# Performance work log

Measured on AMD Instinct MI355X. Metric: run time of the kernel, lower is better.

Reference implementation:

```python
import jax, jax.numpy as jnp
import numpy as np

N = 262144  # points per batch (~4096 rays x 64 samples)
FDIM = 64   # plane feature dim
S = 512     # base plane resolution


def setup_inputs() -> dict:
    key = jax.random.key(0)
    ks = jax.random.split(key, 10)
    x = jax.random.uniform(ks[0], (N, 3), dtype=jnp.float32, minval=-1.0, maxval=1.0)
    rays_o = jnp.array([[0.0, 0.0, 1.5]], dtype=jnp.float32)  # ray origin; distances straddle 1.5/2.0
    scale = jnp.ones((3,), dtype=jnp.float32)
    plane = lambda k, s: jax.random.normal(k, (FDIM, s, s), dtype=jnp.float32)
    return {
        'x': x, 'rays_o': rays_o, 'scale': scale,
        'xy_plane': plane(ks[1], S), 'yz_plane': plane(ks[2], S), 'xz_plane': plane(ks[3], S),
        'xy_plane1': plane(ks[4], S // 2), 'yz_plane1': plane(ks[5], S // 2), 'xz_plane1': plane(ks[6], S // 2),
        'xy_plane2': plane(ks[7], S // 4), 'yz_plane2': plane(ks[8], S // 4), 'xz_plane2': plane(ks[9], S // 4),
    }


def bilinear_sample(plane, coords):
    """F.grid_sample(mode='bilinear', align_corners=True, padding_mode='zeros').
    plane: [C, H, W]; coords: [N, 2] with (x, y) in [-1, 1] (x indexes W).
    Returns [N, C]."""
    C, H, W = plane.shape
    fx = (coords[:, 0] + 1.0) * 0.5 * (W - 1)
    fy = (coords[:, 1] + 1.0) * 0.5 * (H - 1)
    x0 = jnp.floor(fx)
    y0 = jnp.floor(fy)
    wx = fx - x0
    wy = fy - y0
    x0i = x0.astype(jnp.int32)
    y0i = y0.astype(jnp.int32)

    def gather(xi, yi):
        valid = (xi >= 0) & (xi < W) & (yi >= 0) & (yi < H)
        xc = jnp.clip(xi, 0, W - 1)
        yc = jnp.clip(yi, 0, H - 1)
        v = plane[:, yc, xc]  # [C, N]
        return jnp.where(valid[None, :], v, 0.0)

    v00 = gather(x0i, y0i)
    v01 = gather(x0i + 1, y0i)
    v10 = gather(x0i, y0i + 1)
    v11 = gather(x0i + 1, y0i + 1)
    out = (v00 * (1 - wx) * (1 - wy) + v01 * wx * (1 - wy)
           + v10 * (1 - wx) * wy + v11 * wx * wy)  # [C, N]
    return out.T


def forward(x, rays_o, scale, xy0, yz0, xz0, xy1, yz1, xz1, xy2, yz2, xz2):
    xs = x * scale[None, :]
    xy_c = xs[:, :2]                                   # (x, y)
    xz_c = jnp.stack([xs[:, 0], xs[:, 2]], axis=-1)    # (x, z)
    yz_c = xs[:, 1:]                                   # (y, z)

    # laplace breakpoints: first index with distance > 1.5 / > 2.0 from rays_o[0]
    d = jnp.linalg.norm(rays_o[0][None, :] - xs, axis=-1)
    c1 = d > 1.5
    c2 = d > 2.0
    break1 = jnp.where(c1.any(), jnp.argmax(c1), 0)
    break2 = jnp.where(c2.any(), jnp.argmax(c2), 0)
    idx = jnp.arange(x.shape[0])
    # level 0: [0, break1), level 1: [break1, break2), level 2: [break2, N)
    level = jnp.where(idx < break1, 0, jnp.where(idx < break2, 1, 2))[:, None]

    def tri(p0, p1, p2, c):
        s0 = bilinear_sample(p0, c)
        s1 = bilinear_sample(p1, c)
        s2 = bilinear_sample(p2, c)
        # laplace: level1 = fine + half, level2 = fine + half + quarter
        return jnp.where(level == 0, s0, jnp.where(level == 1, s0 + s1, s0 + s1 + s2))

    return (tri(xy0, xy1, xy2, xy_c)
            + tri(xz0, xz1, xz2, xz_c)
            + tri(yz0, yz1, yz2, yz_c))


def reference(x, rays_o, scale, xy_plane, yz_plane, xz_plane, xy_plane1, yz_plane1, xz_plane1, xy_plane2, yz_plane2, xz_plane2):
    return forward(x, rays_o, scale, xy_plane, yz_plane, xz_plane,
                   xy_plane1, yz_plane1, xz_plane1,
                   xy_plane2, yz_plane2, xz_plane2)
```

## Files before the change

kernel.cpp:

```cpp
#include <hip/hip_runtime.h>
#include <hip/hip_fp16.h>

#define NPTS 262144
#define FDIM 64
#define NCELL 4096

typedef float vfloat4 __attribute__((ext_vector_type(4)));

__global__ __launch_bounds__(256) void break_kernel(const float* __restrict__ x,
                                                    const float* __restrict__ rays_o,
                                                    const float* __restrict__ scale,
                                                    unsigned* __restrict__ breaks) {
  const unsigned t = blockIdx.x * 256u + threadIdx.x;
  const float r0 = rays_o[0], r1 = rays_o[1], r2 = rays_o[2];
  const float s0 = scale[0], s1 = scale[1], s2 = scale[2];
  unsigned b1 = 0xFFFFFFFFu, b2 = 0xFFFFFFFFu;
  for (unsigned p = t; p < NPTS; p += 65536u) {
    const float dx = r0 - x[p * 3 + 0] * s0;
    const float dy = r1 - x[p * 3 + 1] * s1;
    const float dz = r2 - x[p * 3 + 2] * s2;
    const float d = sqrtf(__fadd_rn(__fadd_rn(__fmul_rn(dx, dx), __fmul_rn(dy, dy)),
                                    __fmul_rn(dz, dz)));
    if (d > 1.5f) b1 = min(b1, p);
    if (d > 2.0f) b2 = min(b2, p);
  }
#pragma unroll
  for (int o = 32; o > 0; o >>= 1) {
    b1 = min(b1, (unsigned)__shfl_down((int)b1, o, 64));
    b2 = min(b2, (unsigned)__shfl_down((int)b2, o, 64));
  }
  if ((threadIdx.x & 63) == 0) {
    atomicMin(&breaks[0], b1);
    atomicMin(&breaks[1], b2);
  }
}

__device__ __forceinline__ unsigned part4(unsigned v) {
  v &= 15u;
  v = (v | (v << 4)) & 0x0C3u;
  v = (v | (v << 2)) & 0x249u;
  return v;
}

__device__ __forceinline__ unsigned cell_key(float x0, float x1, float x2) {
  const int cx = min(max((int)((x0 + 1.0f) * 8.0f), 0), 15);
  const int cy = min(max((int)((x1 + 1.0f) * 8.0f), 0), 15);
  const int cz = min(max((int)((x2 + 1.0f) * 8.0f), 0), 15);
  return part4((unsigned)cx) | (part4((unsigned)cy) << 1) | (part4((unsigned)cz) << 2);
}

#define NB_BH (NPTS / 256)
#define TPIX 128

struct TransposeArgs {
  const float* src[9];
  __half* dst[9];
  int tile_hi[9];
  int SS[9];
};

union H8 { uint4 u; __half h[8]; };

__global__ __launch_bounds__(256) void fused_bh_transpose(const float* __restrict__ x,
                                                          const float* __restrict__ rays_o,
                                                          const float* __restrict__ scale,
                                                          unsigned* __restrict__ breaks,
                                                          unsigned* __restrict__ hist,
                                                          TransposeArgs a) {
  const int bid = blockIdx.x;
  if (bid < NB_BH) {
    const unsigned t = (unsigned)bid * 256u + threadIdx.x;
    const float s0 = scale[0], s1 = scale[1], s2 = scale[2];
    const float xs0 = x[t * 3 + 0] * s0;
    const float xs1 = x[t * 3 + 1] * s1;
    const float xs2 = x[t * 3 + 2] * s2;
    const float dx = rays_o[0] - xs0;
    const float dy = rays_o[1] - xs1;
    const float dz = rays_o[2] - xs2;
    const float d = sqrtf(__fadd_rn(__fadd_rn(__fmul_rn(dx, dx), __fmul_rn(dy, dy)),
                                    __fmul_rn(dz, dz)));
    unsigned m1 = (d > 1.5f) ? (NPTS - t) : 0u;
    unsigned m2 = (d > 2.0f) ? (NPTS - t) : 0u;
#pragma unroll
    for (int o = 32; o > 0; o >>= 1) {
      m1 = max(m1, (unsigned)__shfl_down((int)m1, o, 64));
      m2 = max(m2, (unsigned)__shfl_down((int)m2, o, 64));
    }
    if ((threadIdx.x & 63) == 0) {
      atomicMax(&breaks[0], m1);
      atomicMax(&breaks[1], m2);
    }
    const unsigned key = cell_key(xs0, xs1, xs2);
    atomicAdd(&hist[key], 1u);
    return;
  }
  const int tile = bid - NB_BH;
  int pi = 0;
#pragma unroll
  for (int i = 0; i < 9; ++i) {
    if (tile >= a.tile_hi[i]) pi = i + 1;
  }
  const int lo = (pi == 0) ? 0 : a.tile_hi[pi - 1];
  const float* __restrict__ src = a.src[pi];
  __half* __restrict__ dst = a.dst[pi];
  const size_t SS = (size_t)a.SS[pi];

  const int ntm = (int)(SS / TPIX) - 1;
  const int tl = ((tile - lo) * 997) & ntm;

  const int t = threadIdx.x;
  const int slot = t >> 3;
  const int c8 = t & 7;
  const size_t p0 = (size_t)tl * TPIX + (size_t)slot * 4;
  const float* __restrict__ srcb = src + (size_t)(c8 * 8) * SS + p0;

  H8 h[4];
#pragma unroll
  for (int k = 0; k < 8; ++k) {
    const float4 v = *(const float4*)(srcb + (size_t)k * SS);
    h[0].h[k] = __float2half(v.x);
    h[1].h[k] = __float2half(v.y);
    h[2].h[k] = __float2half(v.z);
    h[3].h[k] = __float2half(v.w);
  }
#pragma unroll
  for (int r = 0; r < 4; ++r) {
    *(uint4*)(dst + (p0 + (size_t)r) * FDIM + c8 * 8) = h[r].u;
  }
}

__global__ __launch_bounds__(1024) void scan_kernel(unsigned* __restrict__ hist) {
  const int tid = threadIdx.x;
  uint4 h = ((uint4*)hist)[tid];
  const unsigned i0 = h.x;
  const unsigned i1 = i0 + h.y;
  const unsigned i2 = i1 + h.z;
  const unsigned i3 = i2 + h.w;
  __shared__ unsigned ls[1024];
  ls[tid] = i3;
  __syncthreads();
  for (int d = 1; d < 1024; d <<= 1) {
    const unsigned add = (tid >= d) ? ls[tid - d] : 0u;
    __syncthreads();
    ls[tid] += add;
    __syncthreads();
  }
  const unsigned base = ls[tid] - i3;
  uint4 o;
  o.x = base;
  o.y = base + i0;
  o.z = base + i1;
  o.w = base + i2;
  ((uint4*)hist)[tid] = o;
}

__global__ __launch_bounds__(256) void scatter_kernel(const float* __restrict__ x,
                                                      const float* __restrict__ scale,
                                                      const unsigned* __restrict__ breaks,
                                                      unsigned* __restrict__ offs,
                                                      unsigned* __restrict__ order) {
  const unsigned t = blockIdx.x * 256u + threadIdx.x;
  const float s0 = scale[0], s1 = scale[1], s2 = scale[2];
  const float xs0 = x[t * 3 + 0] * s0;
  const float xs1 = x[t * 3 + 1] * s1;
  const float xs2 = x[t * 3 + 2] * s2;
  const unsigned key = cell_key(xs0, xs1, xs2);
  const unsigned pos = atomicAdd(&offs[key], 1u);
  unsigned b1 = NPTS - breaks[0]; if (b1 >= NPTS) b1 = 0;
  unsigned b2 = NPTS - breaks[1]; if (b2 >= NPTS) b2 = 0;
  const unsigned lvl = (t < b1) ? 0u : ((t < b2) ? 1u : 2u);
  order[pos] = t | (lvl << 18);
}

__device__ __forceinline__ void bilinear_weights(int W, float cx, float cy,
                                                 float& w00, float& w01, float& w10, float& w11,
                                                 int& xc0, int& xc1, int& yc0, int& yc1) {
  const float Wm1 = (float)(W - 1);
  const float fx = (cx + 1.0f) * 0.5f * Wm1;
  const float fy = (cy + 1.0f) * 0.5f * Wm1;
  const float x0f = floorf(fx), y0f = floorf(fy);
  const float wx = fx - x0f, wy = fy - y0f;
  const int ix = (int)x0f, iy = (int)y0f;
  const int ix1 = ix + 1, iy1 = iy + 1;
  const bool vx0 = (ix >= 0) && (ix < W);
  const bool vx1 = (ix1 >= 0) && (ix1 < W);
  const bool vy0 = (iy >= 0) && (iy < W);
  const bool vy1 = (iy1 >= 0) && (iy1 < W);
  xc0 = min(max(ix, 0), W - 1);
  xc1 = min(max(ix1, 0), W - 1);
  yc0 = min(max(iy, 0), W - 1);
  yc1 = min(max(iy1, 0), W - 1);
  w00 = (1.0f - wx) * (1.0f - wy) * (float)(vx0 && vy0);
  w01 = wx * (1.0f - wy) * (float)(vx1 && vy0);
  w10 = (1.0f - wx) * wy * (float)(vx0 && vy1);
  w11 = wx * wy * (float)(vx1 && vy1);
}

__device__ __forceinline__ void sample8_t(const __half* __restrict__ pl, int W,
                                          float cx, float cy, int j8, float acc[8]) {
  float w00, w01, w10, w11;
  int xc0, xc1, yc0, yc1;
  bilinear_weights(W, cx, cy, w00, w01, w10, w11, xc0, xc1, yc0, yc1);
  const __half* b00 = pl + ((size_t)(yc0 * W + xc0) * FDIM + j8);
  const __half* b01 = pl + ((size_t)(yc0 * W + xc1) * FDIM + j8);
  const __half* b10 = pl + ((size_t)(yc1 * W + xc0) * FDIM + j8);
  const __half* b11 = pl + ((size_t)(yc1 * W + xc1) * FDIM + j8);
  H8 v00, v01, v10, v11;
  v00.u = *(const uint4*)b00;
  v01.u = *(const uint4*)b01;
  v10.u = *(const uint4*)b10;
  v11.u = *(const uint4*)b11;
#pragma unroll
  for (int k = 0; k < 8; ++k) {
    acc[k] += w00 * __half2float(v00.h[k]) + w01 * __half2float(v01.h[k]) +
              w10 * __half2float(v10.h[k]) + w11 * __half2float(v11.h[k]);
  }
}

__device__ __forceinline__ void sample8_d(const float* __restrict__ pl, int W,
                                          float cx, float cy, int j8, float acc[8]) {
  float w00, w01, w10, w11;
  int xc0, xc1, yc0, yc1;
  bilinear_weights(W, cx, cy, w00, w01, w10, w11, xc0, xc1, yc0, yc1);
  const size_t SS = (size_t)W * W;
  const int i00 = yc0 * W + xc0, i01 = yc0 * W + xc1;
  const int i10 = yc1 * W + xc0, i11 = yc1 * W + xc1;
#pragma unroll
  for (int k = 0; k < 8; ++k) {
    const size_t co = (size_t)(j8 + k) * SS;
    acc[k] += w00 * pl[co + i00] + w01 * pl[co + i01] +
              w10 * pl[co + i10] + w11 * pl[co + i11];
  }
}

struct PlanesH { const __half* p[9]; };
struct PlanesF { const float* p[9]; };

#define SAMPLE_BLOCKS (NPTS * 8 / 256)
#define XCD_CHUNK (SAMPLE_BLOCKS / 8)

__global__ __launch_bounds__(256) void sample_kernel(const float* __restrict__ x,
                                                     const float* __restrict__ scale,
                                                     const unsigned* __restrict__ order,
                                                     PlanesH tp, float* __restrict__ out) {
  const unsigned b = blockIdx.x;
  const unsigned sb = (b & 7u) * XCD_CHUNK + (b >> 3);
  const int t = (int)(sb * 256u + threadIdx.x);
  const int slot = t >> 3;
  const int j8 = (t & 7) * 8;
  const unsigned pk = order[slot];
  const int p = (int)(pk & 0x3FFFFu);
  const int level = (int)(pk >> 18);
  const float s0 = scale[0], s1 = scale[1], s2 = scale[2];
  const float xs0 = x[p * 3 + 0] * s0;
  const float xs1 = x[p * 3 + 1] * s1;
  const float xs2 = x[p * 3 + 2] * s2;
  float acc[8];
#pragma unroll
  for (int k = 0; k < 8; ++k) acc[k] = 0.0f;
  sample8_t(tp.p[0], 512, xs0, xs1, j8, acc);
  sample8_t(tp.p[1], 512, xs1, xs2, j8, acc);
  sample8_t(tp.p[2], 512, xs0, xs2, j8, acc);
  if (level >= 1) {
    sample8_t(tp.p[3], 256, xs0, xs1, j8, acc);
    sample8_t(tp.p[4], 256, xs1, xs2, j8, acc);
    sample8_t(tp.p[5], 256, xs0, xs2, j8, acc);
  }
  if (level >= 2) {
    sample8_t(tp.p[6], 128, xs0, xs1, j8, acc);
    sample8_t(tp.p[7], 128, xs1, xs2, j8, acc);
    sample8_t(tp.p[8], 128, xs0, xs2, j8, acc);
  }
  float* o = out + (size_t)p * FDIM + j8;
  vfloat4 lo = {acc[0], acc[1], acc[2], acc[3]};
  vfloat4 hi = {acc[4], acc[5], acc[6], acc[7]};
  __builtin_nontemporal_store(lo, (vfloat4*)o);
  __builtin_nontemporal_store(hi, (vfloat4*)(o + 4));
}

__global__ __launch_bounds__(256) void sample_kernel_direct(const float* __restrict__ x,
                                                            const float* __restrict__ scale,
                                                            const unsigned* __restrict__ breaks,
                                                            PlanesF tp, float* __restrict__ out) {
  const int t = blockIdx.x * 256 + threadIdx.x;
  const int p = t >> 3;
  const int j8 = (t & 7) * 8;
  const float s0 = scale[0], s1 = scale[1], s2 = scale[2];
  const float xs0 = x[p * 3 + 0] * s0;
  const float xs1 = x[p * 3 + 1] * s1;
  const float xs2 = x[p * 3 + 2] * s2;
  unsigned b1 = breaks[0]; if (b1 >= NPTS) b1 = 0;
  unsigned b2 = breaks[1]; if (b2 >= NPTS) b2 = 0;
  const unsigned pu = (unsigned)p;
  const int level = (pu < b1) ? 0 : ((pu < b2) ? 1 : 2);
  float acc[8];
#pragma unroll
  for (int k = 0; k < 8; ++k) acc[k] = 0.0f;
  sample8_d(tp.p[0], 512, xs0, xs1, j8, acc);
  sample8_d(tp.p[1], 512, xs1, xs2, j8, acc);
  sample8_d(tp.p[2], 512, xs0, xs2, j8, acc);
  if (level >= 1) {
    sample8_d(tp.p[3], 256, xs0, xs1, j8, acc);
    sample8_d(tp.p[4], 256, xs1, xs2, j8, acc);
    sample8_d(tp.p[5], 256, xs0, xs2, j8, acc);
  }
  if (level >= 2) {
    sample8_d(tp.p[6], 128, xs0, xs1, j8, acc);
    sample8_d(tp.p[7], 128, xs1, xs2, j8, acc);
    sample8_d(tp.p[8], 128, xs0, xs2, j8, acc);
  }
  float4* o4 = (float4*)(out + (size_t)p * FDIM + j8);
  o4[0] = make_float4(acc[0], acc[1], acc[2], acc[3]);
  o4[1] = make_float4(acc[4], acc[5], acc[6], acc[7]);
}

extern "C" void kernel_launch(void* const* d_in, const int* in_sizes, int n_in,
                              void* d_out, int out_size, void* d_ws, size_t ws_size,
                              hipStream_t stream) {
  const float* x = (const float*)d_in[0];
  const float* rays_o = (const float*)d_in[1];
  const float* scale = (const float*)d_in[2];
  const float* pl32[9];
  for (int i = 0; i < 9; ++i) pl32[i] = (const float*)d_in[3 + i];
  float* out = (float*)d_out;

  unsigned char* ws = (unsigned char*)d_ws;
  unsigned* breaks = (unsigned*)ws;
  unsigned* hist = (unsigned*)(ws + 256);
  unsigned* order = (unsigned*)(ws + 256 + NCELL * 4);
  const size_t planes_off = 256 + (size_t)NCELL * 4 + (size_t)NPTS * 4;

  const int Ss[3] = {512, 256, 128};
  size_t need = planes_off;
  for (int l = 0; l < 3; ++l) need += 3 * (size_t)Ss[l] * Ss[l] * FDIM * sizeof(__half);

  if (ws_size >= need) {
    (void)hipMemsetAsync(d_ws, 0, 256 + NCELL * 4, stream);

    PlanesH tp;
    TransposeArgs ta;
    size_t off = planes_off;
    int tiles_acc = 0;
    for (int l = 0; l < 3; ++l) {
      const int S = Ss[l];
      const int SS = S * S;
      for (int o = 0; o < 3; ++o) {
        const int i = l * 3 + o;
        __half* dst = (__half*)(ws + off);
        tp.p[i] = dst;
        ta.src[i] = pl32[i];
        ta.dst[i] = dst;
        ta.SS[i] = SS;
        tiles_acc += SS / TPIX;
        ta.tile_hi[i] = tiles_acc;
        off += (size_t)SS * FDIM * sizeof(__half);
      }
    }
    fused_bh_transpose<<<NB_BH + tiles_acc, 256, 0, stream>>>(x, rays_o, scale,
                                                              breaks, hist, ta);
    scan_kernel<<<1, 1024, 0, stream>>>(hist);
    scatter_kernel<<<NPTS / 256, 256, 0, stream>>>(x, scale, breaks, hist, order);
    sample_kernel<<<SAMPLE_BLOCKS, 256, 0, stream>>>(x, scale, order, tp, out);
  } else {
    (void)hipMemsetAsync(d_ws, 0xFF, 8, stream);
    break_kernel<<<256, 256, 0, stream>>>(x, rays_o, scale, breaks);
    PlanesF tf;
    for (int i = 0; i < 9; ++i) tf.p[i] = pl32[i];
    sample_kernel_direct<<<(NPTS * 8) / 256, 256, 0, stream>>>(x, scale, breaks, tf, out);
  }
}
```

Before: 474.9 us.

## Replace global-atomic counting sort with per-block LDS histograms and split transpose

The binning of points into Morton cells now uses 64 blocks, each building a shared-memory histogram and storing cell keys. A scan kernel sums the per-block histograms, prefix-scans them and writes per-block offsets. Scatter then reuses the stored keys and applies LDS atomics instead of global ones. The plane transpose is split out of the fused kernel into its own launch after the sort. This removes global atomic contention on the histogram, but the sort now runs on only 64 blocks and the serial scan over blocks lengthens the critical path.

```diff
diff --git a/kernel.cpp b/kernel.cpp
--- a/kernel.cpp
+++ b/kernel.cpp
@@ -4,6 +4,8 @@
 #define NPTS 262144
 #define FDIM 64
 #define NCELL 4096
+#define NBLK 64
+#define PPT 16
 
 typedef float vfloat4 __attribute__((ext_vector_type(4)));
 
@@ -49,93 +51,61 @@
   return part4((unsigned)cx) | (part4((unsigned)cy) << 1) | (part4((unsigned)cz) << 2);
 }
 
-#define NB_BH (NPTS / 256)
-#define TPIX 128
-
-struct TransposeArgs {
-  const float* src[9];
-  __half* dst[9];
-  int tile_hi[9];
-  int SS[9];
-};
-
-union H8 { uint4 u; __half h[8]; };
-
-__global__ __launch_bounds__(256) void fused_bh_transpose(const float* __restrict__ x,
-                                                          const float* __restrict__ rays_o,
-                                                          const float* __restrict__ scale,
-                                                          unsigned* __restrict__ breaks,
-                                                          unsigned* __restrict__ hist,
-                                                          TransposeArgs a) {
-  const int bid = blockIdx.x;
-  if (bid < NB_BH) {
-    const unsigned t = (unsigned)bid * 256u + threadIdx.x;
-    const float s0 = scale[0], s1 = scale[1], s2 = scale[2];
-    const float xs0 = x[t * 3 + 0] * s0;
-    const float xs1 = x[t * 3 + 1] * s1;
-    const float xs2 = x[t * 3 + 2] * s2;
-    const float dx = rays_o[0] - xs0;
-    const float dy = rays_o[1] - xs1;
-    const float dz = rays_o[2] - xs2;
+__global__ __launch_bounds__(256) void bh_hist_kernel(const float* __restrict__ x,
+                                                      const float* __restrict__ rays_o,
+                                                      const float* __restrict__ scale,
+                                                      unsigned* __restrict__ breaks,
+                                                      unsigned short* __restrict__ keys,
+                                                      unsigned* __restrict__ blockhist) {
+  __shared__ unsigned lh[NCELL];
+  for (int i = threadIdx.x; i < NCELL; i += 256) lh[i] = 0u;
+  __syncthreads();
+  const float r0 = rays_o[0], r1 = rays_o[1], r2 = rays_o[2];
+  const float s0 = scale[0], s1 = scale[1], s2 = scale[2];
+  const unsigned base = blockIdx.x * 256u + threadIdx.x;
+  unsigned m1 = 0u, m2 = 0u;
+#pragma unroll
+  for (int k = 0; k < PPT; ++k) {
+    const unsigned p = base + (unsigned)k * (NBLK * 256u);
+    const float xs0 = x[p * 3 + 0] * s0;
+    const float xs1 = x[p * 3 + 1] * s1;
+    const float xs2 = x[p * 3 + 2] * s2;
+    const float dx = r0 - xs0;
+    const float dy = r1 - xs1;
+    const float dz = r2 - xs2;
     const float d = sqrtf(__fadd_rn(__fadd_rn(__fmul_rn(dx, dx), __fmul_rn(dy, dy)),
                                     __fmul_rn(dz, dz)));
-    unsigned m1 = (d > 1.5f) ? (NPTS - t) : 0u;
-    unsigned m2 = (d > 2.0f) ? (NPTS - t) : 0u;
-#pragma unroll
-    for (int o = 32; o > 0; o >>= 1) {
-      m1 = max(m1, (unsigned)__shfl_down((int)m1, o, 64));
-      m2 = max(m2, (unsigned)__shfl_down((int)m2, o, 64));
-    }
-    if ((threadIdx.x & 63) == 0) {
-      atomicMax(&breaks[0], m1);
-      atomicMax(&breaks[1], m2);
-    }
+    if (d > 1.5f) m1 = max(m1, NPTS - p);
+    if (d > 2.0f) m2 = max(m2, NPTS - p);
     const unsigned key = cell_key(xs0, xs1, xs2);
-    atomicAdd(&hist[key], 1u);
-    return;
-  }
-  const int tile = bid - NB_BH;
-  int pi = 0;
-#pragma unroll
-  for (int i = 0; i < 9; ++i) {
-    if (tile >= a.tile_hi[i]) pi = i + 1;
-  }
-  const int lo = (pi == 0) ? 0 : a.tile_hi[pi - 1];
-  const float* __restrict__ src = a.src[pi];
-  __half* __restrict__ dst = a.dst[pi];
-  const size_t SS = (size_t)a.SS[pi];
-
-  const int ntm = (int)(SS / TPIX) - 1;
-  const int tl = ((tile - lo) * 997) & ntm;
-
-  const int t = threadIdx.x;
-  const int slot = t >> 3;
-  const int c8 = t & 7;
-  const size_t p0 = (size_t)tl * TPIX + (size_t)slot * 4;
-  const float* __restrict__ srcb = src + (size_t)(c8 * 8) * SS + p0;
-
-  H8 h[4];
-#pragma unroll
-  for (int k = 0; k < 8; ++k) {
-    const float4 v = *(const float4*)(srcb + (size_t)k * SS);
-    h[0].h[k] = __float2half(v.x);
-    h[1].h[k] = __float2half(v.y);
-    h[2].h[k] = __float2half(v.z);
-    h[3].h[k] = __float2half(v.w);
-  }
-#pragma unroll
-  for (int r = 0; r < 4; ++r) {
-    *(uint4*)(dst + (p0 + (size_t)r) * FDIM + c8 * 8) = h[r].u;
-  }
-}
-
-__global__ __launch_bounds__(1024) void scan_kernel(unsigned* __restrict__ hist) {
+    atomicAdd(&lh[key], 1u);
+    keys[p] = (unsigned short)key;
+  }
+#pragma unroll
+  for (int o = 32; o > 0; o >>= 1) {
+    m1 = max(m1, (unsigned)__shfl_down((int)m1, o, 64));
+    m2 = max(m2, (unsigned)__shfl_down((int)m2, o, 64));
+  }
+  if ((threadIdx.x & 63) == 0) {
+    atomicMax(&breaks[0], m1);
+    atomicMax(&breaks[1], m2);
+  }
+  __syncthreads();
+  unsigned* bh = blockhist + (size_t)blockIdx.x * NCELL;
+  for (int i = threadIdx.x; i < NCELL; i += 256) bh[i] = lh[i];
+}
+
+__global__ __launch_bounds__(1024) void scan_kernel(unsigned* __restrict__ blockhist) {
   const int tid = threadIdx.x;
-  uint4 h = ((uint4*)hist)[tid];
-  const unsigned i0 = h.x;
-  const unsigned i1 = i0 + h.y;
-  const unsigned i2 = i1 + h.z;
-  const unsigned i3 = i2 + h.w;
+  uint4 acc = make_uint4(0u, 0u, 0u, 0u);
+  for (int b = 0; b < NBLK; ++b) {
+    const uint4 v = ((const uint4*)(blockhist + (size_t)b * NCELL))[tid];
+    acc.x += v.x; acc.y += v.y; acc.z += v.z; acc.w += v.w;
+  }
+  const unsigned i0 = acc.x;
+  const unsigned i1 = i0 + acc.y;
+  const unsigned i2 = i1 + acc.z;
+  const unsigned i3 = i2 + acc.w;
   __shared__ unsigned ls[1024];
   ls[tid] = i3;
   __syncthreads();
@@ -146,30 +116,85 @@
     __syncthreads();
   }
   const unsigned base = ls[tid] - i3;
-  uint4 o;
-  o.x = base;
-  o.y = base + i0;
-  o.z = base + i1;
-  o.w = base + i2;
-  ((uint4*)hist)[tid] = o;
-}
-
-__global__ __launch_bounds__(256) void scatter_kernel(const float* __restrict__ x,
-                                                      const float* __restrict__ scale,
+  uint4 run;
+  run.x = base;
+  run.y = base + i0;
+  run.z = base + i1;
+  run.w = base + i2;
+  for (int b = 0; b < NBLK; ++b) {
+    uint4* ptr = (uint4*)(blockhist + (size_t)b * NCELL) + tid;
+    const uint4 v = *ptr;
+    *ptr = run;
+    run.x += v.x; run.y += v.y; run.z += v.z; run.w += v.w;
+  }
+}
+
+__global__ __launch_bounds__(256) void scatter_kernel(const unsigned short* __restrict__ keys,
                                                       const unsigned* __restrict__ breaks,
-                                                      unsigned* __restrict__ offs,
+                                                      const unsigned* __restrict__ blockhist,
                                                       unsigned* __restrict__ order) {
-  const unsigned t = blockIdx.x * 256u + threadIdx.x;
-  const float s0 = scale[0], s1 = scale[1], s2 = scale[2];
-  const float xs0 = x[t * 3 + 0] * s0;
-  const float xs1 = x[t * 3 + 1] * s1;
-  const float xs2 = x[t * 3 + 2] * s2;
-  const unsigned key = cell_key(xs0, xs1, xs2);
-  const unsigned pos = atomicAdd(&offs[key], 1u);
-  unsigned b1 = NPTS - breaks[0]; if (b1 >= NPTS) b1 = 0;
-  unsigned b2 = NPTS - breaks[1]; if (b2 >= NPTS) b2 = 0;
-  const unsigned lvl = (t < b1) ? 0u : ((t < b2) ? 1u : 2u);
-  order[pos] = t | (lvl << 18);
+  __shared__ unsigned lh[NCELL];
+  const unsigned* bh = blockhist + (size_t)blockIdx.x * NCELL;
+  for (int i = threadIdx.x; i < NCELL; i += 256) lh[i] = bh[i];
+  __syncthreads();
+  unsigned b1 = NPTS - breaks[0]; if (b1 >= NPTS) b1 = 0u;
+  unsigned b2 = NPTS - breaks[1]; if (b2 >= NPTS) b2 = 0u;
+  const unsigned base = blockIdx.x * 256u + threadIdx.x;
+#pragma unroll
+  for (int k = 0; k < PPT; ++k) {
+    const unsigned p = base + (unsigned)k * (NBLK * 256u);
+    const unsigned key = keys[p];
+    const unsigned pos = atomicAdd(&lh[key], 1u);
+    const unsigned lvl = (p < b1) ? 0u : ((p < b2) ? 1u : 2u);
+    order[pos] = p | (lvl << 18);
+  }
+}
+
+#define TPIX 128
+
+struct TransposeArgs {
+  const float* src[9];
+  __half* dst[9];
+  int tile_hi[9];
+  int SS[9];
+};
+
+union H8 { uint4 u; __half h[8]; };
+
+__global__ __launch_bounds__(256) void transpose_all(TransposeArgs a) {
+  const int tile = blockIdx.x;
+  int pi = 0;
+#pragma unroll
+  for (int i = 0; i < 9; ++i) {
+    if (tile >= a.tile_hi[i]) pi = i + 1;
+  }
+  const int lo = (pi == 0) ? 0 : a.tile_hi[pi - 1];
+  const float* __restrict__ src = a.src[pi];
+  __half* __restrict__ dst = a.dst[pi];
+  const size_t SS = (size_t)a.SS[pi];
+
+  const int ntm = (int)(SS / TPIX) - 1;
+  const int tl = ((tile - lo) * 997) & ntm;
+
+  const int t = threadIdx.x;
+  const int slot = t >> 3;
+  const int c8 = t & 7;
+  const size_t p0 = (size_t)tl * TPIX + (size_t)slot * 4;
+  const float* __restrict__ srcb = src + (size_t)(c8 * 8) * SS + p0;
+
+  H8 h[4];
+#pragma unroll
+  for (int k = 0; k < 8; ++k) {
+    const float4 v = *(const float4*)(srcb + (size_t)k * SS);
+    h[0].h[k] = __float2half(v.x);
+    h[1].h[k] = __float2half(v.y);
+    h[2].h[k] = __float2half(v.z);
+    h[3].h[k] = __float2half(v.w);
+  }
+#pragma unroll
+  for (int r = 0; r < 4; ++r) {
+    *(uint4*)(dst + (p0 + (size_t)r) * FDIM + c8 * 8) = h[r].u;
+  }
 }
 
 __device__ __forceinline__ void bilinear_weights(int W, float cx, float cy,
@@ -326,16 +351,21 @@
 
   unsigned char* ws = (unsigned char*)d_ws;
   unsigned* breaks = (unsigned*)ws;
-  unsigned* hist = (unsigned*)(ws + 256);
-  unsigned* order = (unsigned*)(ws + 256 + NCELL * 4);
-  const size_t planes_off = 256 + (size_t)NCELL * 4 + (size_t)NPTS * 4;
+  unsigned short* keys = (unsigned short*)(ws + 256);
+  unsigned* blockhist = (unsigned*)(ws + 256 + (size_t)NPTS * 2);
+  unsigned* order = (unsigned*)(ws + 256 + (size_t)NPTS * 2 + (size_t)NBLK * NCELL * 4);
+  const size_t planes_off = 256 + (size_t)NPTS * 2 + (size_t)NBLK * NCELL * 4 + (size_t)NPTS * 4;
 
   const int Ss[3] = {512, 256, 128};
   size_t need = planes_off;
   for (int l = 0; l < 3; ++l) need += 3 * (size_t)Ss[l] * Ss[l] * FDIM * sizeof(__half);
 
   if (ws_size >= need) {
-    (void)hipMemsetAsync(d_ws, 0, 256 + NCELL * 4, stream);
+    (void)hipMemsetAsync(d_ws, 0, 256, stream);
+
+    bh_hist_kernel<<<NBLK, 256, 0, stream>>>(x, rays_o, scale, breaks, keys, blockhist);
+    scan_kernel<<<1, 1024, 0, stream>>>(blockhist);
+    scatter_kernel<<<NBLK, 256, 0, stream>>>(keys, breaks, blockhist, order);
 
     PlanesH tp;
     TransposeArgs ta;
@@ -356,10 +386,7 @@
         off += (size_t)SS * FDIM * sizeof(__half);
       }
     }
-    fused_bh_transpose<<<NB_BH + tiles_acc, 256, 0, stream>>>(x, rays_o, scale,
-                                                              breaks, hist, ta);
-    scan_kernel<<<1, 1024, 0, stream>>>(hist);
-    scatter_kernel<<<NPTS / 256, 256, 0, stream>>>(x, scale, breaks, hist, order);
+    transpose_all<<<tiles_acc, 256, 0, stream>>>(ta);
     sample_kernel<<<SAMPLE_BLOCKS, 256, 0, stream>>>(x, scale, order, tp, out);
   } else {
     (void)hipMemsetAsync(d_ws, 0xFF, 8, stream);
```

Result: faster. 426.4 us (-10.2%).

## Drop spatial sort pipeline and sample points in original order

Applied to the files above, without the earlier changes.

Removes the histogram, scan and scatter kernels that sorted points by Morton cell, so the sample kernel now processes points in their natural index order and computes each point's level directly from the break indices. The break search is folded into fewer blocks, each covering 16 points per thread. This removes two kernel launches and the order buffer traffic, but gives up the gather locality the spatial sort provided, so plane texel accesses become random across the planes.

```diff
diff --git a/kernel.cpp b/kernel.cpp
--- a/kernel.cpp
+++ b/kernel.cpp
@@ -3,53 +3,11 @@
 
 #define NPTS 262144
 #define FDIM 64
-#define NCELL 4096
+#define NBRK 64
+#define BPPT 16
 
 typedef float vfloat4 __attribute__((ext_vector_type(4)));
 
-__global__ __launch_bounds__(256) void break_kernel(const float* __restrict__ x,
-                                                    const float* __restrict__ rays_o,
-                                                    const float* __restrict__ scale,
-                                                    unsigned* __restrict__ breaks) {
-  const unsigned t = blockIdx.x * 256u + threadIdx.x;
-  const float r0 = rays_o[0], r1 = rays_o[1], r2 = rays_o[2];
-  const float s0 = scale[0], s1 = scale[1], s2 = scale[2];
-  unsigned b1 = 0xFFFFFFFFu, b2 = 0xFFFFFFFFu;
-  for (unsigned p = t; p < NPTS; p += 65536u) {
-    const float dx = r0 - x[p * 3 + 0] * s0;
-    const float dy = r1 - x[p * 3 + 1] * s1;
-    const float dz = r2 - x[p * 3 + 2] * s2;
-    const float d = sqrtf(__fadd_rn(__fadd_rn(__fmul_rn(dx, dx), __fmul_rn(dy, dy)),
-                                    __fmul_rn(dz, dz)));
-    if (d > 1.5f) b1 = min(b1, p);
-    if (d > 2.0f) b2 = min(b2, p);
-  }
-#pragma unroll
-  for (int o = 32; o > 0; o >>= 1) {
-    b1 = min(b1, (unsigned)__shfl_down((int)b1, o, 64));
-    b2 = min(b2, (unsigned)__shfl_down((int)b2, o, 64));
-  }
-  if ((threadIdx.x & 63) == 0) {
-    atomicMin(&breaks[0], b1);
-    atomicMin(&breaks[1], b2);
-  }
-}
-
-__device__ __forceinline__ unsigned part4(unsigned v) {
-  v &= 15u;
-  v = (v | (v << 4)) & 0x0C3u;
-  v = (v | (v << 2)) & 0x249u;
-  return v;
-}
-
-__device__ __forceinline__ unsigned cell_key(float x0, float x1, float x2) {
-  const int cx = min(max((int)((x0 + 1.0f) * 8.0f), 0), 15);
-  const int cy = min(max((int)((x1 + 1.0f) * 8.0f), 0), 15);
-  const int cz = min(max((int)((x2 + 1.0f) * 8.0f), 0), 15);
-  return part4((unsigned)cx) | (part4((unsigned)cy) << 1) | (part4((unsigned)cz) << 2);
-}
-
-#define NB_BH (NPTS / 256)
 #define TPIX 128
 
 struct TransposeArgs {
@@ -61,26 +19,28 @@
 
 union H8 { uint4 u; __half h[8]; };
 
-__global__ __launch_bounds__(256) void fused_bh_transpose(const float* __restrict__ x,
-                                                          const float* __restrict__ rays_o,
-                                                          const float* __restrict__ scale,
-                                                          unsigned* __restrict__ breaks,
-                                                          unsigned* __restrict__ hist,
-                                                          TransposeArgs a) {
+__global__ __launch_bounds__(256) void fused_break_transpose(const float* __restrict__ x,
+                                                             const float* __restrict__ rays_o,
+                                                             const float* __restrict__ scale,
+                                                             unsigned* __restrict__ breaks,
+                                                             TransposeArgs a) {
   const int bid = blockIdx.x;
-  if (bid < NB_BH) {
-    const unsigned t = (unsigned)bid * 256u + threadIdx.x;
+  if (bid < NBRK) {
+    const float r0 = rays_o[0], r1 = rays_o[1], r2 = rays_o[2];
     const float s0 = scale[0], s1 = scale[1], s2 = scale[2];
-    const float xs0 = x[t * 3 + 0] * s0;
-    const float xs1 = x[t * 3 + 1] * s1;
-    const float xs2 = x[t * 3 + 2] * s2;
-    const float dx = rays_o[0] - xs0;
-    const float dy = rays_o[1] - xs1;
-    const float dz = rays_o[2] - xs2;
-    const float d = sqrtf(__fadd_rn(__fadd_rn(__fmul_rn(dx, dx), __fmul_rn(dy, dy)),
-                                    __fmul_rn(dz, dz)));
-    unsigned m1 = (d > 1.5f) ? (NPTS - t) : 0u;
-    unsigned m2 = (d > 2.0f) ? (NPTS - t) : 0u;
+    const unsigned pb = (unsigned)bid * 4096u + threadIdx.x;
+    unsigned m1 = 0u, m2 = 0u;
+#pragma unroll
+    for (int k = 0; k < BPPT; ++k) {
+      const unsigned p = pb + (unsigned)k * 256u;
+      const float dx = r0 - x[p * 3 + 0] * s0;
+      const float dy = r1 - x[p * 3 + 1] * s1;
+      const float dz = r2 - x[p * 3 + 2] * s2;
+      const float d = sqrtf(__fadd_rn(__fadd_rn(__fmul_rn(dx, dx), __fmul_rn(dy, dy)),
+                                      __fmul_rn(dz, dz)));
+      if (d > 1.5f) m1 = max(m1, NPTS - p);
+      if (d > 2.0f) m2 = max(m2, NPTS - p);
+    }
 #pragma unroll
     for (int o = 32; o > 0; o >>= 1) {
       m1 = max(m1, (unsigned)__shfl_down((int)m1, o, 64));
@@ -90,11 +50,9 @@
       atomicMax(&breaks[0], m1);
       atomicMax(&breaks[1], m2);
     }
-    const unsigned key = cell_key(xs0, xs1, xs2);
-    atomicAdd(&hist[key], 1u);
     return;
   }
-  const int tile = bid - NB_BH;
+  const int tile = bid - NBRK;
   int pi = 0;
 #pragma unroll
   for (int i = 0; i < 9; ++i) {
@@ -127,49 +85,6 @@
   for (int r = 0; r < 4; ++r) {
     *(uint4*)(dst + (p0 + (size_t)r) * FDIM + c8 * 8) = h[r].u;
   }
-}
-
-__global__ __launch_bounds__(1024) void scan_kernel(unsigned* __restrict__ hist) {
-  const int tid = threadIdx.x;
-  uint4 h = ((uint4*)hist)[tid];
-  const unsigned i0 = h.x;
-  const unsigned i1 = i0 + h.y;
-  const unsigned i2 = i1 + h.z;
-  const unsigned i3 = i2 + h.w;
-  __shared__ unsigned ls[1024];
-  ls[tid] = i3;
-  __syncthreads();
-  for (int d = 1; d < 1024; d <<= 1) {
-    const unsigned add = (tid >= d) ? ls[tid - d] : 0u;
-    __syncthreads();
-    ls[tid] += add;
-    __syncthreads();
-  }
-  const unsigned base = ls[tid] - i3;
-  uint4 o;
-  o.x = base;
-  o.y = base + i0;
-  o.z = base + i1;
-  o.w = base + i2;
-  ((uint4*)hist)[tid] = o;
-}
-
-__global__ __launch_bounds__(256) void scatter_kernel(const float* __restrict__ x,
-                                                      const float* __restrict__ scale,
-                                                      const unsigned* __restrict__ breaks,
-                                                      unsigned* __restrict__ offs,
-                                                      unsigned* __restrict__ order) {
-  const unsigned t = blockIdx.x * 256u + threadIdx.x;
-  const float s0 = scale[0], s1 = scale[1], s2 = scale[2];
-  const float xs0 = x[t * 3 + 0] * s0;
-  const float xs1 = x[t * 3 + 1] * s1;
-  const float xs2 = x[t * 3 + 2] * s2;
-  const unsigned key = cell_key(xs0, xs1, xs2);
-  const unsigned pos = atomicAdd(&offs[key], 1u);
-  unsigned b1 = NPTS - breaks[0]; if (b1 >= NPTS) b1 = 0;
-  unsigned b2 = NPTS - breaks[1]; if (b2 >= NPTS) b2 = 0;
-  const unsigned lvl = (t < b1) ? 0u : ((t < b2) ? 1u : 2u);
-  order[pos] = t | (lvl << 18);
 }
 
 __device__ __forceinline__ void bilinear_weights(int W, float cx, float cy,
@@ -236,25 +151,21 @@
 struct PlanesH { const __half* p[9]; };
 struct PlanesF { const float* p[9]; };
 
-#define SAMPLE_BLOCKS (NPTS * 8 / 256)
-#define XCD_CHUNK (SAMPLE_BLOCKS / 8)
-
 __global__ __launch_bounds__(256) void sample_kernel(const float* __restrict__ x,
                                                      const float* __restrict__ scale,
-                                                     const unsigned* __restrict__ order,
+                                                     const unsigned* __restrict__ breaks,
                                                      PlanesH tp, float* __restrict__ out) {
-  const unsigned b = blockIdx.x;
-  const unsigned sb = (b & 7u) * XCD_CHUNK + (b >> 3);
-  const int t = (int)(sb * 256u + threadIdx.x);
-  const int slot = t >> 3;
+  const int t = blockIdx.x * 256 + threadIdx.x;
+  const int p = t >> 3;
   const int j8 = (t & 7) * 8;
-  const unsigned pk = order[slot];
-  const int p = (int)(pk & 0x3FFFFu);
-  const int level = (int)(pk >> 18);
   const float s0 = scale[0], s1 = scale[1], s2 = scale[2];
   const float xs0 = x[p * 3 + 0] * s0;
   const float xs1 = x[p * 3 + 1] * s1;
   const float xs2 = x[p * 3 + 2] * s2;
+  unsigned b1 = NPTS - breaks[0]; if (b1 >= NPTS) b1 = 0u;
+  unsigned b2 = NPTS - breaks[1]; if (b2 >= NPTS) b2 = 0u;
+  const unsigned pu = (unsigned)p;
+  const int level = (pu < b1) ? 0 : ((pu < b2) ? 1 : 2);
   float acc[8];
 #pragma unroll
   for (int k = 0; k < 8; ++k) acc[k] = 0.0f;
@@ -276,6 +187,34 @@
   vfloat4 hi = {acc[4], acc[5], acc[6], acc[7]};
   __builtin_nontemporal_store(lo, (vfloat4*)o);
   __builtin_nontemporal_store(hi, (vfloat4*)(o + 4));
+}
+
+__global__ __launch_bounds__(256) void break_kernel(const float* __restrict__ x,
+                                                    const float* __restrict__ rays_o,
+                                                    const float* __restrict__ scale,
+                                                    unsigned* __restrict__ breaks) {
+  const unsigned t = blockIdx.x * 256u + threadIdx.x;
+  const float r0 = rays_o[0], r1 = rays_o[1], r2 = rays_o[2];
+  const float s0 = scale[0], s1 = scale[1], s2 = scale[2];
+  unsigned m1 = 0u, m2 = 0u;
+  for (unsigned p = t; p < NPTS; p += 65536u) {
+    const float dx = r0 - x[p * 3 + 0] * s0;
+    const float dy = r1 - x[p * 3 + 1] * s1;
+    const float dz = r2 - x[p * 3 + 2] * s2;
+    const float d = sqrtf(__fadd_rn(__fadd_rn(__fmul_rn(dx, dx), __fmul_rn(dy, dy)),
+                                    __fmul_rn(dz, dz)));
+    if (d > 1.5f) m1 = max(m1, NPTS - p);
+    if (d > 2.0f) m2 = max(m2, NPTS - p);
+  }
+#pragma unroll
+  for (int o = 32; o > 0; o >>= 1) {
+    m1 = max(m1, (unsigned)__shfl_down((int)m1, o, 64));
+    m2 = max(m2, (unsigned)__shfl_down((int)m2, o, 64));
+  }
+  if ((threadIdx.x & 63) == 0) {
+    atomicMax(&breaks[0], m1);
+    atomicMax(&breaks[1], m2);
+  }
 }
 
 __global__ __launch_bounds__(256) void sample_kernel_direct(const float* __restrict__ x,
@@ -289,8 +228,8 @@
   const float xs0 = x[p * 3 + 0] * s0;
   const float xs1 = x[p * 3 + 1] * s1;
   const float xs2 = x[p * 3 + 2] * s2;
-  unsigned b1 = breaks[0]; if (b1 >= NPTS) b1 = 0;
-  unsigned b2 = breaks[1]; if (b2 >= NPTS) b2 = 0;
+  unsigned b1 = NPTS - breaks[0]; if (b1 >= NPTS) b1 = 0u;
+  unsigned b2 = NPTS - breaks[1]; if (b2 >= NPTS) b2 = 0u;
   const unsigned pu = (unsigned)p;
   const int level = (pu < b1) ? 0 : ((pu < b2) ? 1 : 2);
   float acc[8];
@@ -326,16 +265,14 @@
 
   unsigned char* ws = (unsigned char*)d_ws;
   unsigned* breaks = (unsigned*)ws;
-  unsigned* hist = (unsigned*)(ws + 256);
-  unsigned* order = (unsigned*)(ws + 256 + NCELL * 4);
-  const size_t planes_off = 256 + (size_t)NCELL * 4 + (size_t)NPTS * 4;
+  const size_t planes_off = 256;
 
   const int Ss[3] = {512, 256, 128};
   size_t need = planes_off;
   for (int l = 0; l < 3; ++l) need += 3 * (size_t)Ss[l] * Ss[l] * FDIM * sizeof(__half);
 
   if (ws_size >= need) {
-    (void)hipMemsetAsync(d_ws, 0, 256 + NCELL * 4, stream);
+    (void)hipMemsetAsync(d_ws, 0, 256, stream);
 
     PlanesH tp;
     TransposeArgs ta;
@@ -356,16 +293,15 @@
         off += (size_t)SS * FDIM * sizeof(__half);
       }
     }
-    fused_bh_transpose<<<NB_BH + tiles_acc, 256, 0, stream>>>(x, rays_o, scale,
-                                                              breaks, hist, ta);
-    scan_kernel<<<1, 1024, 0, stream>>>(hist);
-    scatter_kernel<<<NPTS / 256, 256, 0, stream>>>(x, scale, breaks, hist, order);
-    sample_kernel<<<SAMPLE_BLOCKS, 256, 0, stream>>>(x, scale, order, tp, out);
+    fused_break_transpose<<<NBRK + tiles_acc, 256, 0, stream>>>(x, rays_o, scale,
+                                                                breaks, ta);
+    sample_kernel<<<(NPTS * 8) / 256, 256, 0, stream>>>(x, scale, breaks, tp, out);
   } else {
-    (void)hipMemsetAsync(d_ws, 0xFF, 8, stream);
-    break_kernel<<<256, 256, 0, stream>>>(x, rays_o, scale, breaks);
+    (void)hipMemsetAsync(d_ws, 0, 8, stream);
+    break_kernel<<<256, 256, 0, stream>>>(x, rays_o, scale, (unsigned*)ws);
     PlanesF tf;
     for (int i = 0; i < 9; ++i) tf.p[i] = pl32[i];
-    sample_kernel_direct<<<(NPTS * 8) / 256, 256, 0, stream>>>(x, scale, breaks, tf, out);
-  }
-}
+    sample_kernel_direct<<<(NPTS * 8) / 256, 256, 0, stream>>>(x, scale, (unsigned*)ws,
+                                                               tf, out);
+  }
+}
```

New measurement: 436.7 us. 1.09x faster.
